# Performance work log

Hardware: AMD Instinct MI355X
Metric: run time of the kernel (lower is better)

Reference implementation:

```python
import jax, jax.numpy as jnp
import numpy as np

B, T, C, H = 4, 4096, 1024, 128

def setup_inputs() -> dict:
    key = jax.random.key(0)
    kx, kq, kk, kv = jax.random.split(key, 4)
    s = 1.0 / np.sqrt(C)
    return {
        "x": jax.random.normal(kx, (B, T, C), dtype=jnp.float32),
        "Wq": jax.random.normal(kq, (C, H), dtype=jnp.float32) * s,
        "Wk": jax.random.normal(kk, (C, H), dtype=jnp.float32) * s,
        "Wv": jax.random.normal(kv, (C, H), dtype=jnp.float32) * s,
    }

def reference(x, Wq, Wk, Wv):
    # x: [B,T,C]; projections to [B,T,H]
    q = jnp.einsum('btc,ch->bth', x, Wq)
    k = jnp.einsum('btc,ch->bth', x, Wk)
    v = jnp.einsum('btc,ch->bth', x, Wv)
    scale = 1.0 / jnp.sqrt(jnp.asarray(H, dtype=x.dtype))
    wei = jnp.einsum('bqh,bkh->bqk', q, k) * scale  # [B,T,T]
    causal = jnp.tril(jnp.ones((T, T), dtype=bool))
    wei = jnp.where(causal, wei, -jnp.inf)
    wei = jax.nn.softmax(wei, axis=-1)
    # dropout p=0.0 -> identity
    out = jnp.einsum('bqk,bkh->bqh', wei, v)
    return out
```

## Files before the change

kernel.cpp:

```cpp
#include <hip/hip_runtime.h>
#include <hip/hip_bf16.h>

#define B_ 4
#define T_ 4096
#define C_ 1024
#define H_ 128
#define SEG_ 16

typedef __attribute__((ext_vector_type(8))) short short8;
typedef __attribute__((ext_vector_type(4))) float f32x4;
typedef __attribute__((ext_vector_type(4))) unsigned short u16x4;

static __device__ __forceinline__ unsigned short f2bf(float f) {
    union { float f; unsigned u; } v; v.f = f;
    unsigned r = v.u + 0x7FFF + ((v.u >> 16) & 1);
    return (unsigned short)(r >> 16);
}

__global__ __launch_bounds__(256) void xb_kernel(const float* __restrict__ x,
                                                 unsigned short* __restrict__ xb) {
#pragma unroll
    for (int p = 0; p < 8; ++p) {
        size_t e = (size_t)blockIdx.x * 2048 + p * 256 + threadIdx.x;
        float4 v = ((const float4*)x)[e];
        u16x4 o;
        o.x = f2bf(v.x); o.y = f2bf(v.y); o.z = f2bf(v.z); o.w = f2bf(v.w);
        ((u16x4*)xb)[e] = o;
    }
}

__global__ void wt_kernel(const float* __restrict__ Wq, const float* __restrict__ Wk,
                          const float* __restrict__ Wv, unsigned short* __restrict__ Wt) {
    __shared__ float tile[64][65];
    int c0 = blockIdx.x * 64, h0 = blockIdx.y * 64, w = blockIdx.z;
    const float* W = (w == 0) ? Wq : (w == 1) ? Wk : Wv;
    unsigned short* dst = Wt + (size_t)w * H_ * C_;
    int tr = threadIdx.x >> 6, tc = threadIdx.x & 63;
#pragma unroll
    for (int p = 0; p < 16; ++p) {
        int r = p * 4 + tr;
        tile[r][tc] = W[(size_t)(c0 + r) * H_ + h0 + tc];
    }
    __syncthreads();
#pragma unroll
    for (int p = 0; p < 16; ++p) {
        int r = p * 4 + tr;
        dst[(size_t)(h0 + r) * C_ + c0 + tc] = f2bf(tile[tc][r]);
    }
}

__global__ __launch_bounds__(256) void proj_kernel(
        const unsigned short* __restrict__ xb, const unsigned short* __restrict__ Wt3,
        unsigned short* __restrict__ Q, unsigned short* __restrict__ K,
        unsigned short* __restrict__ Vt) {
    __shared__ unsigned short Xs[128 * 64];
    __shared__ unsigned short Ws[128 * 64];
    int m0 = blockIdx.x * 128;
    int w = blockIdx.y;
    const unsigned short* Wt = Wt3 + (size_t)w * H_ * C_;
    int tid = threadIdx.x;
    int lane = tid & 63, wid = tid >> 6;
    int wr = wid >> 1, wc = wid & 1;
    int l15 = lane & 15, g = lane >> 4;
    int l7 = l15 & 7;

    f32x4 acc[4][4];
#pragma unroll
    for (int i = 0; i < 4; i++)
#pragma unroll
        for (int j = 0; j < 4; j++) acc[i][j] = (f32x4)0.0f;

    for (int kt = 0; kt < C_ / 64; ++kt) {
        int k0 = kt * 64;
#pragma unroll
        for (int p = 0; p < 4; ++p) {
            int idx = tid + p * 256;
            int r = idx >> 3, c = idx & 7;
            short8 v = *(const short8*)(xb + (size_t)(m0 + r) * C_ + k0 + c * 8);
            *(short8*)&Xs[r * 64 + ((c ^ (r & 7)) << 3)] = v;
        }
#pragma unroll
        for (int p = 0; p < 4; ++p) {
            int idx = tid + p * 256;
            int r = idx >> 3, c = idx & 7;
            short8 v = *(const short8*)(Wt + (size_t)r * C_ + k0 + c * 8);
            *(short8*)&Ws[r * 64 + ((c ^ (r & 7)) << 3)] = v;
        }
        __syncthreads();
#pragma unroll
        for (int kf = 0; kf < 2; ++kf) {
            short8 a[4], bvec[4];
#pragma unroll
            for (int mt = 0; mt < 4; mt++) {
                int row = wr * 64 + mt * 16 + l15;
                a[mt] = *(const short8*)&Xs[row * 64 + (((kf * 4 + g) ^ l7) << 3)];
            }
#pragma unroll
            for (int nt = 0; nt < 4; nt++) {
                int row = wc * 64 + nt * 16 + l15;
                bvec[nt] = *(const short8*)&Ws[row * 64 + (((kf * 4 + g) ^ l7) << 3)];
            }
#pragma unroll
            for (int mt = 0; mt < 4; mt++)
#pragma unroll
                for (int nt = 0; nt < 4; nt++)
                    acc[mt][nt] = __builtin_amdgcn_mfma_f32_16x16x32_bf16(a[mt], bvec[nt], acc[mt][nt], 0, 0, 0);
        }
        __syncthreads();
    }
    if (w < 2) {
        unsigned short* outp = (w == 0) ? Q : K;
#pragma unroll
        for (int mt = 0; mt < 4; mt++)
#pragma unroll
            for (int nt = 0; nt < 4; nt++) {
                int row0 = m0 + wr * 64 + mt * 16 + g * 4;
                int col = wc * 64 + nt * 16 + l15;
#pragma unroll
                for (int ri = 0; ri < 4; ri++)
                    outp[(size_t)(row0 + ri) * H_ + col] = f2bf(acc[mt][nt][ri]);
            }
    } else {
        int b = m0 / T_;
        int tbase = m0 - b * T_;
#pragma unroll
        for (int mt = 0; mt < 4; mt++)
#pragma unroll
            for (int nt = 0; nt < 4; nt++) {
                int t0 = tbase + wr * 64 + mt * 16 + g * 4;
                int col = wc * 64 + nt * 16 + l15;
                u16x4 o;
                o.x = f2bf(acc[mt][nt][0]); o.y = f2bf(acc[mt][nt][1]);
                o.z = f2bf(acc[mt][nt][2]); o.w = f2bf(acc[mt][nt][3]);
                *(u16x4*)&Vt[(size_t)(b * H_ + col) * T_ + t0] = o;
            }
    }
}

__global__ __launch_bounds__(256) void attn_kernel(
        const unsigned short* __restrict__ Q, const unsigned short* __restrict__ K,
        const unsigned short* __restrict__ Vt,
        float* __restrict__ Opart, float* __restrict__ Lpart) {
    int qb = blockIdx.x, seg = blockIdx.y, b = blockIdx.z;
    if (seg * SEG_ > qb) return;
    __shared__ unsigned short KsF[64 * 128];
    __shared__ unsigned short VsF[128 * 64];
    __shared__ unsigned short PsF[4][16 * 64];
    int tid = threadIdx.x, lane = tid & 63, wid = tid >> 6;
    int l15 = lane & 15, g = lane >> 4;
    int l7 = l15 & 7;
    int q0w = qb * 64 + wid * 16;
    const float alpha = 0.08838834764831845f;

    short8 aq[4];
#pragma unroll
    for (int kf = 0; kf < 4; kf++)
        aq[kf] = *(const short8*)(Q + (size_t)(b * T_ + q0w + l15) * H_ + kf * 32 + g * 8);

    f32x4 o[8];
#pragma unroll
    for (int i = 0; i < 8; i++) o[i] = (f32x4)0.0f;
    float l_run[4];
#pragma unroll
    for (int ri = 0; ri < 4; ri++) l_run[ri] = 0.f;

    int kt0 = seg * SEG_;
    int kt_end = min(qb, kt0 + SEG_ - 1);

    short8 kreg[4], vreg[4];
#define LOAD_KV(KT) do { int k0_ = (KT) * 64; \
    _Pragma("unroll") \
    for (int p = 0; p < 4; ++p) { int idx = tid + p * 256; \
        kreg[p] = *(const short8*)(K + (size_t)(b * T_ + k0_ + (idx >> 4)) * H_ + (idx & 15) * 8); } \
    _Pragma("unroll") \
    for (int p = 0; p < 4; ++p) { int idx = tid + p * 256; \
        vreg[p] = *(const short8*)(Vt + (size_t)(b * H_ + (idx >> 3)) * T_ + k0_ + (idx & 7) * 8); } \
    } while (0)

    LOAD_KV(kt0);
    for (int kt = kt0; kt <= kt_end; ++kt) {
        int k0 = kt * 64;
        __syncthreads();
#pragma unroll
        for (int p = 0; p < 4; ++p) {
            int idx = tid + p * 256;
            int r = idx >> 4;
            *(short8*)&KsF[r * 128 + (((idx & 15) ^ (r & 7)) << 3)] = kreg[p];
        }
#pragma unroll
        for (int p = 0; p < 4; ++p) {
            int idx = tid + p * 256;
            int r = idx >> 3;
            *(short8*)&VsF[r * 64 + (((idx & 7) ^ (r & 7)) << 3)] = vreg[p];
        }
        __syncthreads();
        if (kt < kt_end) LOAD_KV(kt + 1);

        f32x4 s[4];
#pragma unroll
        for (int ct = 0; ct < 4; ct++) {
            s[ct] = (f32x4)0.0f;
#pragma unroll
            for (int kf = 0; kf < 4; kf++) {
                int row = ct * 16 + l15;
                short8 bk = *(const short8*)&KsF[row * 128 + (((kf * 4 + g) ^ l7) << 3)];
                s[ct] = __builtin_amdgcn_mfma_f32_16x16x32_bf16(aq[kf], bk, s[ct], 0, 0, 0);
            }
        }
        bool diag = (kt == qb);
#pragma unroll
        for (int ct = 0; ct < 4; ct++)
#pragma unroll
            for (int ri = 0; ri < 4; ri++) {
                float v = s[ct][ri] * alpha;
                if (diag) {
                    int kkg = k0 + ct * 16 + l15;
                    int qg = q0w + g * 4 + ri;
                    if (kkg > qg) v = -1e30f;
                }
                float p = __expf(v);
                l_run[ri] += p;
                int row = g * 4 + ri;
                PsF[wid][row * 64 + (((2 * ct + (l15 >> 3)) ^ (row & 7)) << 3) + l7] = f2bf(p);
            }

#pragma unroll
        for (int kf2 = 0; kf2 < 2; kf2++) {
            short8 ap = *(const short8*)&PsF[wid][l15 * 64 + (((kf2 * 4 + g) ^ l7) << 3)];
#pragma unroll
            for (int ht = 0; ht < 8; ht++) {
                int row = ht * 16 + l15;
                short8 bv = *(const short8*)&VsF[row * 64 + (((kf2 * 4 + g) ^ l7) << 3)];
                o[ht] = __builtin_amdgcn_mfma_f32_16x16x32_bf16(ap, bv, o[ht], 0, 0, 0);
            }
        }
    }
#undef LOAD_KV

    size_t slot = (((size_t)b * (T_ / 64) + qb) * 4 + seg);
    float* Ob = Opart + slot * 64 * 128;
    float* Lb = Lpart + slot * 64;
#pragma unroll
    for (int ri = 0; ri < 4; ri++) {
        float l = l_run[ri];
#pragma unroll
        for (int off = 1; off < 16; off <<= 1)
            l += __shfl_xor(l, off, 64);
        int qrow = wid * 16 + g * 4 + ri;
        Lb[qrow] = l;
#pragma unroll
        for (int ht = 0; ht < 8; ht++)
            Ob[(size_t)qrow * 128 + ht * 16 + l15] = o[ht][ri];
    }
}

__global__ __launch_bounds__(256) void combine_kernel(
        const float* __restrict__ Opart, const float* __restrict__ Lpart,
        float* __restrict__ out) {
    int qt = blockIdx.x, b = blockIdx.y;
    int nseg = qt / SEG_ + 1;
    int tid = threadIdx.x;
    size_t obase = (((size_t)b * (T_ / 64) + qt) * 4) * 64 * 128;
    size_t lbase = (((size_t)b * (T_ / 64) + qt) * 4) * 64;
    float4* dst = (float4*)(out + ((size_t)b * T_ + qt * 64) * 128);
#pragma unroll
    for (int i = 0; i < 8; ++i) {
        int e4 = tid + i * 256;
        int q = e4 >> 5;
        float4 acc = {0.f, 0.f, 0.f, 0.f};
        float lsum = 0.f;
        for (int s = 0; s < nseg; ++s) {
            float4 v = *((const float4*)(Opart + obase + (size_t)s * 64 * 128) + e4);
            acc.x += v.x; acc.y += v.y; acc.z += v.z; acc.w += v.w;
            lsum += Lpart[lbase + s * 64 + q];
        }
        float inv = 1.0f / lsum;
        float4 r = {acc.x * inv, acc.y * inv, acc.z * inv, acc.w * inv};
        dst[e4] = r;
    }
}

extern "C" void kernel_launch(void* const* d_in, const int* in_sizes, int n_in,
                              void* d_out, int out_size, void* d_ws, size_t ws_size,
                              hipStream_t stream) {
    const float* x  = (const float*)d_in[0];
    const float* Wq = (const float*)d_in[1];
    const float* Wk = (const float*)d_in[2];
    const float* Wv = (const float*)d_in[3];
    float* out = (float*)d_out;

    unsigned short* Wt = (unsigned short*)d_ws;
    unsigned short* xbp = Wt + 3 * (size_t)H_ * C_;
    unsigned short* Qb = xbp + (size_t)B_ * T_ * C_;
    unsigned short* Kb = Qb + (size_t)B_ * T_ * H_;
    unsigned short* Vt = Kb + (size_t)B_ * T_ * H_;
    float* Opart = (float*)(Vt + (size_t)B_ * T_ * H_);
    float* Lpart = Opart + (size_t)B_ * 64 * 4 * 64 * 128;

    xb_kernel<<<dim3((B_ * T_ * C_ / 4) / 2048), 256, 0, stream>>>(x, xbp);
    wt_kernel<<<dim3(C_ / 64, H_ / 64, 3), 256, 0, stream>>>(Wq, Wk, Wv, Wt);
    proj_kernel<<<dim3((B_ * T_) / 128, 3), 256, 0, stream>>>(xbp, Wt, Qb, Kb, Vt);
    attn_kernel<<<dim3(T_ / 64, 4, B_), 256, 0, stream>>>(Qb, Kb, Vt, Opart, Lpart);
    combine_kernel<<<dim3(T_ / 64, B_), 256, 0, stream>>>(Opart, Lpart, out);
}
```

Measured before the change: 199.2 us.

## Fuse x bf16 conversion into QKV projection and split attention into more segments

Removes the separate x-to-bf16 kernel and its intermediate buffer; the projection kernel now reads fp32 x directly, converts in registers, and computes all three Q/K/V outputs in one block of 32 rows, loading weight fragments straight from global memory instead of LDS. The attention split-K segment count doubles (SEG 16->8, grid y 4->8) to raise parallelism on long causal rows, with combine and workspace indexing updated. This saves a full read and write of bf16 x, but weights are reloaded from global/L2 by every block with no LDS reuse, and combine must merge more partials.

After: 215.7 us. 1.08x slower.

```diff
diff --git a/kernel.cpp b/kernel.cpp
--- a/kernel.cpp
+++ b/kernel.cpp
@@ -5,7 +5,7 @@
 #define T_ 4096
 #define C_ 1024
 #define H_ 128
-#define SEG_ 16
+#define SEG_ 8
 
 typedef __attribute__((ext_vector_type(8))) short short8;
 typedef __attribute__((ext_vector_type(4))) float f32x4;
@@ -15,18 +15,6 @@
     union { float f; unsigned u; } v; v.f = f;
     unsigned r = v.u + 0x7FFF + ((v.u >> 16) & 1);
     return (unsigned short)(r >> 16);
-}
-
-__global__ __launch_bounds__(256) void xb_kernel(const float* __restrict__ x,
-                                                 unsigned short* __restrict__ xb) {
-#pragma unroll
-    for (int p = 0; p < 8; ++p) {
-        size_t e = (size_t)blockIdx.x * 2048 + p * 256 + threadIdx.x;
-        float4 v = ((const float4*)x)[e];
-        u16x4 o;
-        o.x = f2bf(v.x); o.y = f2bf(v.y); o.z = f2bf(v.z); o.w = f2bf(v.w);
-        ((u16x4*)xb)[e] = o;
-    }
 }
 
 __global__ void wt_kernel(const float* __restrict__ Wq, const float* __restrict__ Wk,
@@ -50,90 +38,80 @@
 }
 
 __global__ __launch_bounds__(256) void proj_kernel(
-        const unsigned short* __restrict__ xb, const unsigned short* __restrict__ Wt3,
+        const float* __restrict__ x, const unsigned short* __restrict__ Wt3,
         unsigned short* __restrict__ Q, unsigned short* __restrict__ K,
         unsigned short* __restrict__ Vt) {
-    __shared__ unsigned short Xs[128 * 64];
-    __shared__ unsigned short Ws[128 * 64];
-    int m0 = blockIdx.x * 128;
-    int w = blockIdx.y;
-    const unsigned short* Wt = Wt3 + (size_t)w * H_ * C_;
+    __shared__ unsigned short Xs[32 * 64];
+    int m0 = blockIdx.x * 32;
     int tid = threadIdx.x;
     int lane = tid & 63, wid = tid >> 6;
-    int wr = wid >> 1, wc = wid & 1;
     int l15 = lane & 15, g = lane >> 4;
     int l7 = l15 & 7;
 
-    f32x4 acc[4][4];
-#pragma unroll
-    for (int i = 0; i < 4; i++)
-#pragma unroll
-        for (int j = 0; j < 4; j++) acc[i][j] = (f32x4)0.0f;
+    f32x4 acc[2][6];
+#pragma unroll
+    for (int i = 0; i < 2; i++)
+#pragma unroll
+        for (int j = 0; j < 6; j++) acc[i][j] = (f32x4)0.0f;
 
     for (int kt = 0; kt < C_ / 64; ++kt) {
         int k0 = kt * 64;
-#pragma unroll
-        for (int p = 0; p < 4; ++p) {
-            int idx = tid + p * 256;
-            int r = idx >> 3, c = idx & 7;
-            short8 v = *(const short8*)(xb + (size_t)(m0 + r) * C_ + k0 + c * 8);
-            *(short8*)&Xs[r * 64 + ((c ^ (r & 7)) << 3)] = v;
-        }
-#pragma unroll
-        for (int p = 0; p < 4; ++p) {
-            int idx = tid + p * 256;
-            int r = idx >> 3, c = idx & 7;
-            short8 v = *(const short8*)(Wt + (size_t)r * C_ + k0 + c * 8);
-            *(short8*)&Ws[r * 64 + ((c ^ (r & 7)) << 3)] = v;
+        {
+            int r = tid >> 3, c8 = tid & 7;
+            const float* src = x + (size_t)(m0 + r) * C_ + k0 + c8 * 8;
+            float4 v0 = *(const float4*)src;
+            float4 v1 = *(const float4*)(src + 4);
+            union { short8 s; u16x4 h[2]; } pk;
+            pk.h[0].x = f2bf(v0.x); pk.h[0].y = f2bf(v0.y);
+            pk.h[0].z = f2bf(v0.z); pk.h[0].w = f2bf(v0.w);
+            pk.h[1].x = f2bf(v1.x); pk.h[1].y = f2bf(v1.y);
+            pk.h[1].z = f2bf(v1.z); pk.h[1].w = f2bf(v1.w);
+            *(short8*)&Xs[r * 64 + ((c8 ^ (r & 7)) << 3)] = pk.s;
         }
         __syncthreads();
 #pragma unroll
         for (int kf = 0; kf < 2; ++kf) {
-            short8 a[4], bvec[4];
-#pragma unroll
-            for (int mt = 0; mt < 4; mt++) {
-                int row = wr * 64 + mt * 16 + l15;
+            short8 a[2], bv[6];
+#pragma unroll
+            for (int mt = 0; mt < 2; mt++) {
+                int row = mt * 16 + l15;
                 a[mt] = *(const short8*)&Xs[row * 64 + (((kf * 4 + g) ^ l7) << 3)];
             }
 #pragma unroll
-            for (int nt = 0; nt < 4; nt++) {
-                int row = wc * 64 + nt * 16 + l15;
-                bvec[nt] = *(const short8*)&Ws[row * 64 + (((kf * 4 + g) ^ l7) << 3)];
-            }
-#pragma unroll
-            for (int mt = 0; mt < 4; mt++)
-#pragma unroll
-                for (int nt = 0; nt < 4; nt++)
-                    acc[mt][nt] = __builtin_amdgcn_mfma_f32_16x16x32_bf16(a[mt], bvec[nt], acc[mt][nt], 0, 0, 0);
-        }
-        __syncthreads();
-    }
-    if (w < 2) {
-        unsigned short* outp = (w == 0) ? Q : K;
-#pragma unroll
-        for (int mt = 0; mt < 4; mt++)
-#pragma unroll
-            for (int nt = 0; nt < 4; nt++) {
-                int row0 = m0 + wr * 64 + mt * 16 + g * 4;
-                int col = wc * 64 + nt * 16 + l15;
+            for (int nt = 0; nt < 6; nt++) {
+                int r = wid * 96 + nt * 16 + l15;
+                bv[nt] = *(const short8*)(Wt3 + (size_t)r * C_ + k0 + (kf * 4 + g) * 8);
+            }
+#pragma unroll
+            for (int mt = 0; mt < 2; mt++)
+#pragma unroll
+                for (int nt = 0; nt < 6; nt++)
+                    acc[mt][nt] = __builtin_amdgcn_mfma_f32_16x16x32_bf16(a[mt], bv[nt], acc[mt][nt], 0, 0, 0);
+        }
+        __syncthreads();
+    }
+    int b = m0 >> 12;
+    int tbase = m0 & (T_ - 1);
+#pragma unroll
+    for (int nt = 0; nt < 6; nt++) {
+        int col = wid * 96 + nt * 16 + l15;
+        int w = col >> 7, h = col & 127;
+#pragma unroll
+        for (int mt = 0; mt < 2; mt++) {
+            if (w < 2) {
+                unsigned short* outp = (w == 0) ? Q : K;
+                int row0 = m0 + mt * 16 + g * 4;
 #pragma unroll
                 for (int ri = 0; ri < 4; ri++)
-                    outp[(size_t)(row0 + ri) * H_ + col] = f2bf(acc[mt][nt][ri]);
-            }
-    } else {
-        int b = m0 / T_;
-        int tbase = m0 - b * T_;
-#pragma unroll
-        for (int mt = 0; mt < 4; mt++)
-#pragma unroll
-            for (int nt = 0; nt < 4; nt++) {
-                int t0 = tbase + wr * 64 + mt * 16 + g * 4;
-                int col = wc * 64 + nt * 16 + l15;
+                    outp[(size_t)(row0 + ri) * H_ + h] = f2bf(acc[mt][nt][ri]);
+            } else {
+                int t0 = tbase + mt * 16 + g * 4;
                 u16x4 o;
                 o.x = f2bf(acc[mt][nt][0]); o.y = f2bf(acc[mt][nt][1]);
                 o.z = f2bf(acc[mt][nt][2]); o.w = f2bf(acc[mt][nt][3]);
-                *(u16x4*)&Vt[(size_t)(b * H_ + col) * T_ + t0] = o;
-            }
+                *(u16x4*)&Vt[(size_t)(b * H_ + h) * T_ + t0] = o;
+            }
+        }
     }
 }
 
@@ -237,7 +215,7 @@
     }
 #undef LOAD_KV
 
-    size_t slot = (((size_t)b * (T_ / 64) + qb) * 4 + seg);
+    size_t slot = (((size_t)b * (T_ / 64) + qb) * 8 + seg);
     float* Ob = Opart + slot * 64 * 128;
     float* Lb = Lpart + slot * 64;
 #pragma unroll
@@ -260,8 +238,8 @@
     int qt = blockIdx.x, b = blockIdx.y;
     int nseg = qt / SEG_ + 1;
     int tid = threadIdx.x;
-    size_t obase = (((size_t)b * (T_ / 64) + qt) * 4) * 64 * 128;
-    size_t lbase = (((size_t)b * (T_ / 64) + qt) * 4) * 64;
+    size_t obase = (((size_t)b * (T_ / 64) + qt) * 8) * 64 * 128;
+    size_t lbase = (((size_t)b * (T_ / 64) + qt) * 8) * 64;
     float4* dst = (float4*)(out + ((size_t)b * T_ + qt * 64) * 128);
 #pragma unroll
     for (int i = 0; i < 8; ++i) {
@@ -290,16 +268,14 @@
     float* out = (float*)d_out;
 
     unsigned short* Wt = (unsigned short*)d_ws;
-    unsigned short* xbp = Wt + 3 * (size_t)H_ * C_;
-    unsigned short* Qb = xbp + (size_t)B_ * T_ * C_;
+    unsigned short* Qb = Wt + 3 * (size_t)H_ * C_;
     unsigned short* Kb = Qb + (size_t)B_ * T_ * H_;
     unsigned short* Vt = Kb + (size_t)B_ * T_ * H_;
     float* Opart = (float*)(Vt + (size_t)B_ * T_ * H_);
-    float* Lpart = Opart + (size_t)B_ * 64 * 4 * 64 * 128;
-
-    xb_kernel<<<dim3((B_ * T_ * C_ / 4) / 2048), 256, 0, stream>>>(x, xbp);
+    float* Lpart = Opart + (size_t)B_ * 64 * 8 * 64 * 128;
+
     wt_kernel<<<dim3(C_ / 64, H_ / 64, 3), 256, 0, stream>>>(Wq, Wk, Wv, Wt);
-    proj_kernel<<<dim3((B_ * T_) / 128, 3), 256, 0, stream>>>(xbp, Wt, Qb, Kb, Vt);
-    attn_kernel<<<dim3(T_ / 64, 4, B_), 256, 0, stream>>>(Qb, Kb, Vt, Opart, Lpart);
+    proj_kernel<<<dim3((B_ * T_) / 32), 256, 0, stream>>>(x, Wt, Qb, Kb, Vt);
+    attn_kernel<<<dim3(T_ / 64, 8, B_), 256, 0, stream>>>(Qb, Kb, Vt, Opart, Lpart);
     combine_kernel<<<dim3(T_ / 64, B_), 256, 0, stream>>>(Opart, Lpart, out);
 }
```
